# Kernel tuning notes

Measured on AMD Instinct MI355X. Metric: run time of the kernel, lower is better.

The kernel has to match this reference:

```python
import jax, jax.numpy as jnp
import numpy as np
import math

N_MAX, L_MAX, M_MAX = 3, 2, 2

def basis_list(N, L, M):
    out = []
    for n in range(1, N + 1):
        for l in range(0, min(n, L + 1)):
            for m in range(-l, l + 1):
                if abs(m) <= M:
                    out.append((n, l, m))
    return out

BASIS = basis_list(N_MAX, L_MAX, M_MAX)  # 14 (n,l,m) triples


def assoc_laguerre(k, alpha, x):
    # Generalized Laguerre L_k^alpha(x), static small k, via recurrence.
    L0 = jnp.ones_like(x)
    if k == 0:
        return L0
    L1 = (1.0 + alpha) - x
    if k == 1:
        return L1
    for i in range(1, k):
        L2 = (((2 * i + 1 + alpha) - x) * L1 - (i + alpha) * L0) / (i + 1)
        L0, L1 = L1, L2
    return L1


def assoc_legendre(l, m, x):
    # P_l^m(x) for m >= 0 with Condon-Shortley phase, static l, m.
    pmm = jnp.ones_like(x)
    if m > 0:
        somx2 = jnp.sqrt(jnp.maximum(1.0 - x * x, 0.0))
        fact = 1.0
        for _ in range(m):
            pmm = pmm * (-fact) * somx2
            fact += 2.0
    if l == m:
        return pmm
    pmmp1 = x * (2 * m + 1) * pmm
    if l == m + 1:
        return pmmp1
    for ll in range(m + 2, l + 1):
        pll = ((2 * ll - 1) * x * pmmp1 - (ll + m - 1) * pmm) / (ll - m)
        pmm, pmmp1 = pmmp1, pll
    return pmmp1


def real_sph_harm(l, m, cos_theta, phi):
    am = abs(m)
    norm = math.sqrt((2 * l + 1) / (4.0 * math.pi)
                     * math.factorial(l - am) / math.factorial(l + am))
    P = assoc_legendre(l, am, cos_theta)
    if m == 0:
        return norm * P
    if m > 0:
        return math.sqrt(2.0) * norm * P * jnp.cos(am * phi)
    return math.sqrt(2.0) * norm * P * jnp.sin(am * phi)


def radial(n, l, r):
    # Hydrogen radial part R_nl(r) with a0 = 1.
    norm = math.sqrt((2.0 / n) ** 3
                     * math.factorial(n - l - 1)
                     / (2.0 * n * math.factorial(n + l)))
    rho = (2.0 / n) * r
    out = norm * jnp.exp(-0.5 * rho) * assoc_laguerre(n - l - 1, 2 * l + 1, rho)
    if l > 0:
        out = out * rho ** l
    return out


def setup_inputs() -> dict:
    key = jax.random.key(0)
    k1, k2 = jax.random.split(key)
    position = jax.random.uniform(k1, (2048, 4096, 3), dtype=jnp.float32)
    coeffs = jax.random.normal(k2, (len(BASIS),), dtype=jnp.float32)
    return {"position": position, "coeffs": coeffs}


def reference(position, coeffs):
    # position: (OutN, n, 3) = (r, theta, phi) -> output (OutN, n)
    r = position[..., 0]
    theta = position[..., 1]
    phi = position[..., 2]
    ct = jnp.cos(theta)
    out = jnp.zeros(r.shape, dtype=position.dtype)
    for k, (nq, l, m) in enumerate(BASIS):
        psi = radial(nq, l, r) * real_sph_harm(l, m, ct, phi)
        out = out + coeffs[k] * psi
    return out
```

## Files before the change

kernel.cpp:

```cpp
#include <hip/hip_runtime.h>
#include <hip/hip_bf16.h>


__device__ __forceinline__ float eval_point(float r, float theta, float phi,
                                            const float* __restrict__ c) {
    float st, ct;
    __sincosf(theta, &st, &ct);
    float sp, cp;
    __sincosf(phi, &sp, &cp);
    const float s2p = 2.0f * sp * cp;
    const float c2p = 2.0f * cp * cp - 1.0f;

    const float ex  = __expf(r * (-1.0f / 6.0f));
    const float ex2 = ex * ex;
    const float ex3 = ex2 * ex;
    const float e1  = ex3 * ex3;
    const float e2  = ex3;
    const float e3  = ex2;

    const float R10 = 2.0f * e1;
    const float R20 = 0.35355339059f * e2 * (2.0f - r);
    const float R21 = 0.20412414523f * e2 * r;
    const float R30 = 0.12830005982f * e3 * (3.0f + r * (-2.0f + 0.22222222222f * r));
    const float R31 = 0.04536092116f * e3 * r * (2.66666666667f - 0.44444444444f * r);
    const float R32 = 0.00901600915f * e3 * r * r;

    float acc = 0.28209479177f * (c[0] * R10 + c[1] * R20 + c[5] * R30);
    acc += 0.48860251190f * ct * (c[3] * R21 + c[7] * R31);
    acc -= 0.48860251190f * st * (sp * (c[2] * R21 + c[6] * R31)
                                + cp * (c[4] * R21 + c[8] * R31));
    const float y20 = 0.94617469575f * ct * ct - 0.31539156525f;
    acc += R32 * (c[11] * y20
                  - 1.09254843059f * ct * st * (c[10] * sp + c[12] * cp)
                  + 0.54627421529f * st * st * (c[9] * s2p + c[13] * c2p));
    return acc;
}

__global__ __launch_bounds__(256) void orbitals_lds(
    const float4* __restrict__ pos4,
    const float* __restrict__ coeffs,
    float4* __restrict__ out4)
{
    __shared__ float4 smem[768];
    const int t = threadIdx.x;
    const int base4 = blockIdx.x * 768;

#pragma unroll
    for (int k = 0; k < 3; ++k)
        smem[k * 256 + t] = pos4[base4 + k * 256 + t];
    __syncthreads();

    const float4 a = smem[3 * t + 0];
    const float4 b = smem[3 * t + 1];
    const float4 d = smem[3 * t + 2];

    float4 o;
    o.x = eval_point(a.x, a.y, a.z, coeffs);
    o.y = eval_point(a.w, b.x, b.y, coeffs);
    o.z = eval_point(b.z, b.w, d.x, coeffs);
    o.w = eval_point(d.y, d.z, d.w, coeffs);
    out4[blockIdx.x * 256 + t] = o;
}

__global__ void orbitals_tail(
    const float* __restrict__ pos,
    const float* __restrict__ coeffs,
    float* __restrict__ out,
    int start, int total)
{
    const int i = start + blockIdx.x * blockDim.x + threadIdx.x;
    if (i >= total) return;
    out[i] = eval_point(pos[3 * i + 0], pos[3 * i + 1], pos[3 * i + 2], coeffs);
}

extern "C" void kernel_launch(void* const* d_in, const int* in_sizes, int n_in,
                              void* d_out, int out_size, void* d_ws, size_t ws_size,
                              hipStream_t stream) {
    const float* pos    = (const float*)d_in[0];
    const float* coeffs = (const float*)d_in[1];
    float* out = (float*)d_out;

    const int total = out_size;
    const int full_blocks = total / 1024;
    const int done = full_blocks * 1024;
    const int rem = total - done;

    if (full_blocks > 0) {
        orbitals_lds<<<full_blocks, 256, 0, stream>>>(
            (const float4*)pos, coeffs, (float4*)out);
    }
    if (rem > 0) {
        const int block = 256;
        const int grid = (rem + block - 1) / block;
        orbitals_tail<<<grid, block, 0, stream>>>(pos, coeffs, out, done, total);
    }
}
```

Baseline: 153.3 us.

## Use per-wave async global-to-LDS loads with split waits and nontemporal stores

Each wave now loads its own slice of positions straight into LDS with global_load_lds, so the block-wide barrier goes away. It waits on partial vmcnt so it can compute the first half while the second half is still loading. Each thread processes two float4 outputs, so blocks cover 2048 points, and results are written with nontemporal stores. Coefficients are preloaded into registers. The risk is correctness of the hand-written waitcnt ordering for LDS-DMA loads, and fewer blocks in flight.

```diff
diff --git a/kernel.cpp b/kernel.cpp
--- a/kernel.cpp
+++ b/kernel.cpp
@@ -1,6 +1,12 @@
 #include <hip/hip_runtime.h>
-#include <hip/hip_bf16.h>
 
+
+typedef float f32x4 __attribute__((ext_vector_type(4)));
+
+#define GLD_LDS16(gptr, lptr)                                                  \
+    __builtin_amdgcn_global_load_lds(                                          \
+        (const __attribute__((address_space(1))) void*)(gptr),                 \
+        (__attribute__((address_space(3))) void*)(lptr), 16, 0, 0)
 
 __device__ __forceinline__ float eval_point(float r, float theta, float phi,
                                             const float* __restrict__ c) {
@@ -36,30 +42,58 @@
     return acc;
 }
 
-__global__ __launch_bounds__(256) void orbitals_lds(
+__global__ __launch_bounds__(256) void orbitals_wave(
     const float4* __restrict__ pos4,
     const float* __restrict__ coeffs,
     float4* __restrict__ out4)
 {
-    __shared__ float4 smem[768];
-    const int t = threadIdx.x;
-    const int base4 = blockIdx.x * 768;
+    __shared__ float4 smem[1536];
+    const int t    = threadIdx.x;
+    const int lane = t & 63;
+    const int w    = t >> 6;
+
+    float c[14];
+#pragma unroll
+    for (int k = 0; k < 14; ++k) c[k] = coeffs[k];
+
+    const float4* gsrc = pos4 + (size_t)blockIdx.x * 1536 + w * 384 + lane;
+    float4* ldst = &smem[w * 384];
 
 #pragma unroll
-    for (int k = 0; k < 3; ++k)
-        smem[k * 256 + t] = pos4[base4 + k * 256 + t];
-    __syncthreads();
+    for (int j = 0; j < 6; ++j)
+        GLD_LDS16(gsrc + j * 64, ldst + j * 64);
 
-    const float4 a = smem[3 * t + 0];
-    const float4 b = smem[3 * t + 1];
-    const float4 d = smem[3 * t + 2];
+    const int outBase = blockIdx.x * 512 + w * 128 + lane;
+    const int rbase   = w * 384 + 3 * lane;
+    f32x4* __restrict__ outv = (f32x4*)out4;
 
-    float4 o;
-    o.x = eval_point(a.x, a.y, a.z, coeffs);
-    o.y = eval_point(a.w, b.x, b.y, coeffs);
-    o.z = eval_point(b.z, b.w, d.x, coeffs);
-    o.w = eval_point(d.y, d.z, d.w, coeffs);
-    out4[blockIdx.x * 256 + t] = o;
+    asm volatile("s_waitcnt vmcnt(3)" ::: "memory");
+    __builtin_amdgcn_sched_barrier(0);
+    {
+        const float4 a = smem[rbase + 0];
+        const float4 b = smem[rbase + 1];
+        const float4 d = smem[rbase + 2];
+        f32x4 o;
+        o.x = eval_point(a.x, a.y, a.z, c);
+        o.y = eval_point(a.w, b.x, b.y, c);
+        o.z = eval_point(b.z, b.w, d.x, c);
+        o.w = eval_point(d.y, d.z, d.w, c);
+        __builtin_nontemporal_store(o, &outv[outBase]);
+    }
+
+    asm volatile("s_waitcnt vmcnt(1)" ::: "memory");
+    __builtin_amdgcn_sched_barrier(0);
+    {
+        const float4 a = smem[rbase + 192 + 0];
+        const float4 b = smem[rbase + 192 + 1];
+        const float4 d = smem[rbase + 192 + 2];
+        f32x4 o;
+        o.x = eval_point(a.x, a.y, a.z, c);
+        o.y = eval_point(a.w, b.x, b.y, c);
+        o.z = eval_point(b.z, b.w, d.x, c);
+        o.w = eval_point(d.y, d.z, d.w, c);
+        __builtin_nontemporal_store(o, &outv[outBase + 64]);
+    }
 }
 
 __global__ void orbitals_tail(
@@ -81,12 +115,12 @@
     float* out = (float*)d_out;
 
     const int total = out_size;
-    const int full_blocks = total / 1024;
-    const int done = full_blocks * 1024;
+    const int full_blocks = total / 2048;
+    const int done = full_blocks * 2048;
     const int rem = total - done;
 
     if (full_blocks > 0) {
-        orbitals_lds<<<full_blocks, 256, 0, stream>>>(
+        orbitals_wave<<<full_blocks, 256, 0, stream>>>(
             (const float4*)pos, coeffs, (float4*)out);
     }
     if (rem > 0) {
```

Result: no change. 155.7 us (+1.5%).
